# Optimization experiments

Measured on AMD Instinct MI355X. Metric: run time of the kernel, lower is better.

The kernel has to match this reference:

```python
import jax, jax.numpy as jnp
import numpy as np
from jax import lax

V, T, E, H, K = 100000, 4096, 256, 512, 32
Hh = H // 2  # per-direction LSTM hidden


def setup_inputs() -> dict:
    ks = jax.random.split(jax.random.key(0), 16)
    def rn(i, shape, scale=0.1):
        return jax.random.normal(ks[i], shape, dtype=jnp.float32) * scale
    return {
        "sent": jax.random.randint(ks[0], (T,), 0, V),
        "embed": rn(1, (V, E)),
        "Wih_f": rn(2, (4 * Hh, E)), "Whh_f": rn(3, (4 * Hh, Hh)),
        "bih_f": rn(4, (4 * Hh,)), "bhh_f": rn(5, (4 * Hh,)),
        "Wih_b": rn(6, (4 * Hh, E)), "Whh_b": rn(7, (4 * Hh, Hh)),
        "bih_b": rn(8, (4 * Hh,)), "bhh_b": rn(9, (4 * Hh,)),
        "h0": rn(10, (2, Hh)), "c0": rn(11, (2, Hh)),
        "W_out": rn(12, (K, H)), "b_out": rn(13, (K,)),
        "transitions": rn(14, (K, K)),
    }


def _lstm_dir(x, h0, c0, Wih, Whh, bih, bhh):
    # x: (T, E) -> hs: (T, Hh). PyTorch LSTM gate order: i, f, g, o.
    def step(carry, xt):
        h, c = carry
        g = xt @ Wih.T + h @ Whh.T + bih + bhh  # (4*Hh,)
        i, f, gg, o = jnp.split(g, 4)
        c = jax.nn.sigmoid(f) * c + jax.nn.sigmoid(i) * jnp.tanh(gg)
        h = jax.nn.sigmoid(o) * jnp.tanh(c)
        return (h, c), h
    _, hs = lax.scan(step, (h0, c0), x)
    return hs


def _feats(sent, embed, Wih_f, Whh_f, bih_f, bhh_f, Wih_b, Whh_b, bih_b, bhh_b, h0, c0, W_out, b_out):
    x = embed[sent]                                              # (T, E)
    hf = _lstm_dir(x, h0[0], c0[0], Wih_f, Whh_f, bih_f, bhh_f)  # (T, Hh)
    hb = _lstm_dir(x[::-1], h0[1], c0[1], Wih_b, Whh_b, bih_b, bhh_b)[::-1]
    h = jnp.concatenate([hf, hb], axis=-1)                       # (T, H)
    return h @ W_out.T + b_out                                   # (T, K)


def _viterbi(feats, trans):
    # scores[i, j] = prev[i] + trans[i, j] + obs[j]; max/argmax over previous tag i.
    def step(prev, obs):
        scores = prev[:, None] + trans + obs[None, :]  # (K, K)
        best = jnp.max(scores, axis=0)
        ix = jnp.argmax(scores, axis=0)
        return best, (best, ix)
    last, (alphas, ixs) = lax.scan(step, feats[0], feats[1:])
    cur = jnp.argmax(last)
    score = jnp.max(last)
    def back(c, ix_row):
        pre = ix_row[c]
        return pre, pre
    _, prevs = lax.scan(back, cur, ixs, reverse=True)
    path = jnp.concatenate([prevs, cur[None]])  # (T,)
    return path, score


def reference(sent, embed, Wih_f, Whh_f, bih_f, bhh_f, Wih_b, Whh_b, bih_b, bhh_b, h0, c0, W_out, b_out, transitions):
    feats = _feats(sent, embed, Wih_f, Whh_f, bih_f, bhh_f,
                   Wih_b, Whh_b, bih_b, bhh_b, h0, c0, W_out, b_out)
    path, score = _viterbi(feats, transitions)
    return path, score
```

## Files before the change

### kernel.cpp

```cpp
#include <hip/hip_runtime.h>
#include <stdint.h>

#define T_LEN 4096
#define E_DIM 256
#define HH 256

typedef unsigned long long u64;

__device__ __forceinline__ float sigmoidf_(float x) {
    return __builtin_amdgcn_rcpf(1.0f + __expf(-x));
}
__device__ __forceinline__ float tanh_fast(float x) {
    float e = __expf(2.0f * x);
    return 1.0f - 2.0f * __builtin_amdgcn_rcpf(e + 1.0f);
}

template <int CTRL>
__device__ __forceinline__ float dpp_add(float x) {
    int t = __builtin_amdgcn_update_dpp(0, __float_as_int(x), CTRL, 0xF, 0xF, true);
    return x + __int_as_float(t);
}

__global__ __launch_bounds__(256) void proj_kernel(
    const int* __restrict__ sent, const float* __restrict__ embed,
    const float* __restrict__ Wih_f, const float* __restrict__ bih_f, const float* __restrict__ bhh_f,
    const float* __restrict__ Wih_b, const float* __restrict__ bih_b, const float* __restrict__ bhh_b,
    float* __restrict__ gates_f, float* __restrict__ gates_b)
{
    __shared__ float4 xt[16][64];
    const int tid = threadIdx.x;
    const int dir = blockIdx.y;
    const int t0  = blockIdx.x * 16;

    const float* Wih = dir ? Wih_b : Wih_f;
    const float* bih = dir ? bih_b : bih_f;
    const float* bhh = dir ? bhh_b : bhh_f;
    float* gates     = dir ? gates_b : gates_f;

    {
        int row = tid >> 4;
        int c   = tid & 15;
        const float4* src = (const float4*)(embed + (size_t)sent[t0 + row] * E_DIM);
        xt[row][c]      = src[c];
        xt[row][c + 16] = src[c + 16];
        xt[row][c + 32] = src[c + 32];
        xt[row][c + 48] = src[c + 48];
    }
    __syncthreads();

    float acc[4][16];
    #pragma unroll
    for (int ri = 0; ri < 4; ++ri)
        #pragma unroll
        for (int tt = 0; tt < 16; ++tt) acc[ri][tt] = 0.f;

    const float4* wrow0 = (const float4*)(Wih + (size_t)(0 * 256 + tid) * 256);
    const float4* wrow1 = (const float4*)(Wih + (size_t)(1 * 256 + tid) * 256);
    const float4* wrow2 = (const float4*)(Wih + (size_t)(2 * 256 + tid) * 256);
    const float4* wrow3 = (const float4*)(Wih + (size_t)(3 * 256 + tid) * 256);

    for (int k4 = 0; k4 < 64; ++k4) {
        float4 xv[16];
        #pragma unroll
        for (int tt = 0; tt < 16; ++tt) xv[tt] = xt[tt][k4];
        float4 w0 = wrow0[k4], w1 = wrow1[k4], w2 = wrow2[k4], w3 = wrow3[k4];
        #pragma unroll
        for (int tt = 0; tt < 16; ++tt) {
            acc[0][tt] += w0.x*xv[tt].x + w0.y*xv[tt].y + w0.z*xv[tt].z + w0.w*xv[tt].w;
            acc[1][tt] += w1.x*xv[tt].x + w1.y*xv[tt].y + w1.z*xv[tt].z + w1.w*xv[tt].w;
            acc[2][tt] += w2.x*xv[tt].x + w2.y*xv[tt].y + w2.z*xv[tt].z + w2.w*xv[tt].w;
            acc[3][tt] += w3.x*xv[tt].x + w3.y*xv[tt].y + w3.z*xv[tt].z + w3.w*xv[tt].w;
        }
    }

    #pragma unroll
    for (int ri = 0; ri < 4; ++ri) {
        int r = ri * 256 + tid;
        float b = bih[r] + bhh[r];
        #pragma unroll
        for (int tt = 0; tt < 16; ++tt)
            gates[(size_t)(t0 + tt) * 1024 + r] = acc[ri][tt] + b;
    }
}

__global__ __launch_bounds__(512, 1) void lstm_kernel(
    const float* __restrict__ Whh_f, const float* __restrict__ Whh_b,
    const float* __restrict__ gates_f, const float* __restrict__ gates_b,
    const float* __restrict__ h0, const float* __restrict__ c0,
    float* __restrict__ h_out, u64* __restrict__ msg)
{
    const int xcd  = blockIdx.x & 7;
    const int slot = blockIdx.x >> 3;
    if (xcd > 1) return;
    const int dir = xcd;
    const int g   = slot;

    const int tid = threadIdx.x;
    const int jl  = tid >> 4;
    const int s   = tid & 15;
    const int j   = g * 32 + jl;
    const int f   = (s + (s >> 3)) & 7;

    const float* Whh   = dir ? Whh_b : Whh_f;
    const float* gates = dir ? gates_b : gates_f;

    float w[64];
    #pragma unroll
    for (int gg = 0; gg < 4; ++gg) {
        const float2* row2 = (const float2*)(Whh + (size_t)(gg * 256 + j) * 256 + s * 16);
        #pragma unroll
        for (int i = 0; i < 8; ++i) {
            float2 v = row2[(3 * i + f) & 7];
            w[gg * 16 + i * 2 + 0] = v.x;
            w[gg * 16 + i * 2 + 1] = v.y;
        }
    }
    #pragma unroll
    for (int k = 0; k < 64; ++k)
        asm volatile("" : "+a"(w[k]));

    int off[8];
    #pragma unroll
    for (int i = 0; i < 8; ++i)
        off[i] = s * 64 + ((3 * i + f) & 7) * 8;

    __shared__ __align__(16) float h_lds[2][256];

    float c = 0.f;
    if (tid < 32) {
        int j0 = g * 32 + tid;
        float h = h0[dir * HH + j0];
        h_lds[0][j0] = h;
        u64 p = ((u64)1u << 32) | (u64)__float_as_uint(h);
        __hip_atomic_store(&msg[(0 * 2 + dir) * 256 + j0], p,
                           __ATOMIC_RELAXED, __HIP_MEMORY_SCOPE_AGENT);
    }
    if (s <= 1) c = c0[dir * HH + j];

    float gin0 = 0.f, gin1 = 0.f, gin2 = 0.f, gin3 = 0.f;
    if (s <= 1) {
        const int tf0 = dir ? (T_LEN - 1) : 0;
        const float* gp = gates + (size_t)tf0 * 1024 + j;
        gin0 = gp[0]; gin1 = gp[256]; gin2 = gp[512]; gin3 = gp[768];
    }

    for (int t = 0; t < T_LEN; ++t) {
        const int tf = dir ? (T_LEN - 1 - t) : t;

        float ng0 = 0.f, ng1 = 0.f, ng2 = 0.f, ng3 = 0.f;
        if (s <= 1 && t + 1 < T_LEN) {
            const int tfn = dir ? (T_LEN - 2 - t) : (t + 1);
            const float* gp = gates + (size_t)tfn * 1024 + j;
            ng0 = gp[0]; ng1 = gp[256]; ng2 = gp[512]; ng3 = gp[768];
        }

        if (tid < 256 && (tid >> 5) != g) {
            u64* sp = &msg[((t & 1) * 2 + dir) * 256 + tid];
            const unsigned want = (unsigned)(t + 1);
            u64 m;
            do {
                m = __hip_atomic_load(sp, __ATOMIC_RELAXED, __HIP_MEMORY_SCOPE_AGENT);
            } while ((unsigned)(m >> 32) != want);
            h_lds[t & 1][tid] = __uint_as_float((unsigned)m);
        }
        __syncthreads();

        const char* hb = (const char*)(&h_lds[t & 1][0]);
        float p0 = 0.f, p1 = 0.f, p2 = 0.f, p3 = 0.f;
        #pragma unroll
        for (int i = 0; i < 8; ++i) {
            float2 h2 = *(const float2*)(hb + off[i]);
            p0 += w[i*2+0]*h2.x + w[i*2+1]*h2.y;
            p1 += w[16+i*2+0]*h2.x + w[16+i*2+1]*h2.y;
            p2 += w[32+i*2+0]*h2.x + w[32+i*2+1]*h2.y;
            p3 += w[48+i*2+0]*h2.x + w[48+i*2+1]*h2.y;
        }

        p0 = dpp_add<0xB1>(p0);  p1 = dpp_add<0xB1>(p1);
        p2 = dpp_add<0xB1>(p2);  p3 = dpp_add<0xB1>(p3);
        p0 = dpp_add<0x4E>(p0);  p1 = dpp_add<0x4E>(p1);
        p2 = dpp_add<0x4E>(p2);  p3 = dpp_add<0x4E>(p3);
        p0 = dpp_add<0x141>(p0); p1 = dpp_add<0x141>(p1);
        p2 = dpp_add<0x141>(p2); p3 = dpp_add<0x141>(p3);
        p0 = dpp_add<0x140>(p0); p1 = dpp_add<0x140>(p1);
        p2 = dpp_add<0x140>(p2); p3 = dpp_add<0x140>(p3);

        if (s <= 1) {
            float iv = sigmoidf_(gin0 + p0);
            float fv = sigmoidf_(gin1 + p1);
            float gv = tanh_fast(gin2 + p2);
            float ov = sigmoidf_(gin3 + p3);
            c = fv * c + iv * gv;
            float h = ov * tanh_fast(c);
            if (s == 0) {
                u64 pck = ((u64)(unsigned)(t + 2) << 32) | (u64)__float_as_uint(h);
                __hip_atomic_store(&msg[(((t + 1) & 1) * 2 + dir) * 256 + j], pck,
                                   __ATOMIC_RELAXED, __HIP_MEMORY_SCOPE_AGENT);
                h_lds[(t + 1) & 1][j] = h;
            } else {
                h_out[(size_t)tf * 512 + dir * HH + j] = h;
            }
        }
        gin0 = ng0; gin1 = ng1; gin2 = ng2; gin3 = ng3;
    }
}

__global__ __launch_bounds__(64) void feats_kernel(
    const float* __restrict__ h_out, const float* __restrict__ W_out,
    const float* __restrict__ b_out, float* __restrict__ feats)
{
    const int t = blockIdx.x;
    const int lane = threadIdx.x;
    const int k = lane >> 1, half = lane & 1;
    const float4* hv = (const float4*)(h_out + (size_t)t * 512 + half * 256);
    const float4* wv = (const float4*)(W_out + (size_t)k * 512 + half * 256);
    float p = 0.f;
    #pragma unroll 16
    for (int i = 0; i < 64; ++i) {
        float4 a = hv[i], b = wv[i];
        p += a.x*b.x + a.y*b.y + a.z*b.z + a.w*b.w;
    }
    p += __shfl_xor(p, 1);
    if (half == 0) feats[t * 32 + k] = p + b_out[k];
}

#define VT_CHUNK 128
__global__ __launch_bounds__(64) void viterbi_kernel(
    const float* __restrict__ feats, const float* __restrict__ trans,
    float* __restrict__ out)
{
    extern __shared__ unsigned char dynls[];
    unsigned char* ixs = dynls;
    float* fchunk = (float*)(dynls + 131072);
    __shared__ __align__(16) float alf[32];
    __shared__ float fin[32];

    const int lane = threadIdx.x;
    const int j = lane >> 1, ih = lane & 1;

    float ttr[16];
    #pragma unroll
    for (int q = 0; q < 16; ++q) ttr[q] = trans[(ih * 16 + q) * 32 + j];

    float alpha = 0.f;

    for (int cs = 0; cs < T_LEN; cs += VT_CHUNK) {
        const float4* src = (const float4*)(feats + (size_t)cs * 32);
        float4* dst = (float4*)fchunk;
        #pragma unroll
        for (int i = 0; i < 16; ++i) dst[lane + 64 * i] = src[lane + 64 * i];
        __syncthreads();

        int tbeg = cs;
        if (cs == 0) { alpha = fchunk[j]; tbeg = 1; }

        for (int t = tbeg; t < cs + VT_CHUNK; ++t) {
            if (ih == 0) alf[j] = alpha;
            float obs = fchunk[(t - cs) * 32 + j];
            float4 a0 = *(const float4*)&alf[ih * 16 + 0];
            float4 a1 = *(const float4*)&alf[ih * 16 + 4];
            float4 a2 = *(const float4*)&alf[ih * 16 + 8];
            float4 a3 = *(const float4*)&alf[ih * 16 + 12];

            float v[16]; int ix[16];
            v[0]  = a0.x + ttr[0];  v[1]  = a0.y + ttr[1];
            v[2]  = a0.z + ttr[2];  v[3]  = a0.w + ttr[3];
            v[4]  = a1.x + ttr[4];  v[5]  = a1.y + ttr[5];
            v[6]  = a1.z + ttr[6];  v[7]  = a1.w + ttr[7];
            v[8]  = a2.x + ttr[8];  v[9]  = a2.y + ttr[9];
            v[10] = a2.z + ttr[10]; v[11] = a2.w + ttr[11];
            v[12] = a3.x + ttr[12]; v[13] = a3.y + ttr[13];
            v[14] = a3.z + ttr[14]; v[15] = a3.w + ttr[15];
            #pragma unroll
            for (int q = 0; q < 16; ++q) ix[q] = ih * 16 + q;

            #pragma unroll
            for (int st = 8; st >= 1; st >>= 1)
                #pragma unroll
                for (int q = 0; q < 8; ++q)
                    if (q < st && v[q + st] > v[q]) { v[q] = v[q + st]; ix[q] = ix[q + st]; }
            float best = v[0]; int barg = ix[0];

            float ob = __shfl_xor(best, 1); int oa = __shfl_xor(barg, 1);
            float m0 = ih ? ob : best; int a0i = ih ? oa : barg;
            float m1 = ih ? best : ob; int a1i = ih ? barg : oa;
            float m = m0; int a = a0i;
            if (m1 > m0) { m = m1; a = a1i; }
            if (ih == 0) ixs[(t - 1) * 32 + j] = (unsigned char)a;
            alpha = m + obs;
        }
        __syncthreads();
    }

    if (ih == 0) fin[j] = alpha;
    __syncthreads();

    if (lane == 0) {
        float sc = fin[0]; int cur = 0;
        for (int q = 1; q < 32; ++q)
            if (fin[q] > sc) { sc = fin[q]; cur = q; }
        out[T_LEN] = sc;
        out[T_LEN - 1] = (float)cur;
        for (int t = T_LEN - 2; t >= 0; --t) {
            cur = ixs[t * 32 + cur];
            out[t] = (float)cur;
        }
    }
}

extern "C" void kernel_launch(void* const* d_in, const int* in_sizes, int n_in,
                              void* d_out, int out_size, void* d_ws, size_t ws_size,
                              hipStream_t stream) {
    const int*   sent  = (const int*)d_in[0];
    const float* embed = (const float*)d_in[1];
    const float* Wih_f = (const float*)d_in[2];
    const float* Whh_f = (const float*)d_in[3];
    const float* bih_f = (const float*)d_in[4];
    const float* bhh_f = (const float*)d_in[5];
    const float* Wih_b = (const float*)d_in[6];
    const float* Whh_b = (const float*)d_in[7];
    const float* bih_b = (const float*)d_in[8];
    const float* bhh_b = (const float*)d_in[9];
    const float* h0    = (const float*)d_in[10];
    const float* c0    = (const float*)d_in[11];
    const float* W_out = (const float*)d_in[12];
    const float* b_out = (const float*)d_in[13];
    const float* trans = (const float*)d_in[14];
    float* out = (float*)d_out;

    float* gates_f = (float*)d_ws;
    float* gates_b = gates_f + (size_t)T_LEN * 1024;
    float* h_out   = gates_b + (size_t)T_LEN * 1024;
    float* feats   = h_out   + (size_t)T_LEN * 512;
    u64*   msg     = (u64*)(feats + (size_t)T_LEN * 32);

    dim3 gproj(T_LEN / 16, 2);
    proj_kernel<<<gproj, 256, 0, stream>>>(sent, embed,
        Wih_f, bih_f, bhh_f, Wih_b, bih_b, bhh_b, gates_f, gates_b);

    lstm_kernel<<<64, 512, 0, stream>>>(Whh_f, Whh_b, gates_f, gates_b,
                                        h0, c0, h_out, msg);

    feats_kernel<<<T_LEN, 64, 0, stream>>>(h_out, W_out, b_out, feats);

    hipFuncSetAttribute((const void*)viterbi_kernel,
                        hipFuncAttributeMaxDynamicSharedMemorySize, 147456);
    viterbi_kernel<<<1, 64, 147456, stream>>>(feats, trans, out);
}
```

Measured before the change: 5.916 ms.

## Stage LSTM input gates through LDS with a dedicated prefetch wave two steps ahead

Input-gate prefetching moves from per-lane scattered global loads in the gate-computing lanes to a single wave (wave 7). That wave loads the full 1024-float gate row with coalesced float4 loads two timesteps ahead and writes it into a double-buffered LDS array. The gate-computing lanes move from s<=1 to s>=14 and read their gate inputs from LDS. The aim is to take global load latency off the serial recurrence's critical path, at the cost of extra LDS traffic and each block loading the whole row instead of only its own slice.

```diff
diff --git a/kernel.cpp b/kernel.cpp
--- a/kernel.cpp
+++ b/kernel.cpp
@@ -100,6 +100,8 @@
     const int s   = tid & 15;
     const int j   = g * 32 + jl;
     const int f   = (s + (s >> 3)) & 7;
+    const int wv  = tid >> 6;
+    const int lio = tid & 63;
 
     const float* Whh   = dir ? Whh_b : Whh_f;
     const float* gates = dir ? gates_b : gates_f;
@@ -125,6 +127,7 @@
         off[i] = s * 64 + ((3 * i + f) & 7) * 8;
 
     __shared__ __align__(16) float h_lds[2][256];
+    __shared__ __align__(16) float gin_lds[2][1024];
 
     float c = 0.f;
     if (tid < 32) {
@@ -135,24 +138,20 @@
         __hip_atomic_store(&msg[(0 * 2 + dir) * 256 + j0], p,
                            __ATOMIC_RELAXED, __HIP_MEMORY_SCOPE_AGENT);
     }
-    if (s <= 1) c = c0[dir * HH + j];
-
-    float gin0 = 0.f, gin1 = 0.f, gin2 = 0.f, gin3 = 0.f;
-    if (s <= 1) {
-        const int tf0 = dir ? (T_LEN - 1) : 0;
-        const float* gp = gates + (size_t)tf0 * 1024 + j;
-        gin0 = gp[0]; gin1 = gp[256]; gin2 = gp[512]; gin3 = gp[768];
+    if (s >= 14) c = c0[dir * HH + j];
+
+    float4 q0 = {0,0,0,0}, q1 = {0,0,0,0}, q2 = {0,0,0,0}, q3 = {0,0,0,0};
+    if (wv == 7) {
+        const float4* r0 = (const float4*)(gates + (size_t)(dir ? (T_LEN - 1) : 0) * 1024);
+        float4 a0 = r0[lio], a1 = r0[lio + 64], a2 = r0[lio + 128], a3 = r0[lio + 192];
+        float4* gl0 = (float4*)&gin_lds[0][0];
+        gl0[lio] = a0; gl0[lio + 64] = a1; gl0[lio + 128] = a2; gl0[lio + 192] = a3;
+        const float4* r1 = (const float4*)(gates + (size_t)(dir ? (T_LEN - 2) : 1) * 1024);
+        q0 = r1[lio]; q1 = r1[lio + 64]; q2 = r1[lio + 128]; q3 = r1[lio + 192];
     }
 
     for (int t = 0; t < T_LEN; ++t) {
         const int tf = dir ? (T_LEN - 1 - t) : t;
-
-        float ng0 = 0.f, ng1 = 0.f, ng2 = 0.f, ng3 = 0.f;
-        if (s <= 1 && t + 1 < T_LEN) {
-            const int tfn = dir ? (T_LEN - 2 - t) : (t + 1);
-            const float* gp = gates + (size_t)tfn * 1024 + j;
-            ng0 = gp[0]; ng1 = gp[256]; ng2 = gp[512]; ng3 = gp[768];
-        }
 
         if (tid < 256 && (tid >> 5) != g) {
             u64* sp = &msg[((t & 1) * 2 + dir) * 256 + tid];
@@ -185,14 +184,16 @@
         p0 = dpp_add<0x140>(p0); p1 = dpp_add<0x140>(p1);
         p2 = dpp_add<0x140>(p2); p3 = dpp_add<0x140>(p3);
 
-        if (s <= 1) {
+        if (s >= 14) {
+            const float* gl = &gin_lds[t & 1][0];
+            float gin0 = gl[j], gin1 = gl[256 + j], gin2 = gl[512 + j], gin3 = gl[768 + j];
             float iv = sigmoidf_(gin0 + p0);
             float fv = sigmoidf_(gin1 + p1);
             float gv = tanh_fast(gin2 + p2);
             float ov = sigmoidf_(gin3 + p3);
             c = fv * c + iv * gv;
             float h = ov * tanh_fast(c);
-            if (s == 0) {
+            if (s == 15) {
                 u64 pck = ((u64)(unsigned)(t + 2) << 32) | (u64)__float_as_uint(h);
                 __hip_atomic_store(&msg[(((t + 1) & 1) * 2 + dir) * 256 + j], pck,
                                    __ATOMIC_RELAXED, __HIP_MEMORY_SCOPE_AGENT);
@@ -201,7 +202,18 @@
                 h_out[(size_t)tf * 512 + dir * HH + j] = h;
             }
         }
-        gin0 = ng0; gin1 = ng1; gin2 = ng2; gin3 = ng3;
+
+        if (wv == 7) {
+            if (t + 1 < T_LEN) {
+                float4* gl = (float4*)&gin_lds[(t + 1) & 1][0];
+                gl[lio] = q0; gl[lio + 64] = q1; gl[lio + 128] = q2; gl[lio + 192] = q3;
+            }
+            if (t + 2 < T_LEN) {
+                const int tf2 = dir ? (T_LEN - 3 - t) : (t + 2);
+                const float4* r = (const float4*)(gates + (size_t)tf2 * 1024);
+                q0 = r[lio]; q1 = r[lio + 64]; q2 = r[lio + 128]; q3 = r[lio + 192];
+            }
+        }
     }
 }
 
```

Measured after the change: 7.208 ms. 21.8% more time.
